# Optimization experiments

Measured on AMD Instinct MI355X. Metric: run time of the kernel, lower is better.

Reference implementation:

```python
import jax, jax.numpy as jnp
import numpy as np

H = 8          # num query heads
KV = 1         # num kv heads
D = 256        # head_dim
HID = 2048     # hidden_size
B = 4          # sequences in prefill batch
S = 2048       # tokens per sequence
T = B * S      # total tokens
NUM_SLOTS = 16384
ROPE_THETA = 10000.0


def setup_inputs() -> dict:
    key = jax.random.key(0)
    k1, k2, k3 = jax.random.split(key, 3)
    hidden_states = jax.random.normal(k1, (T, HID), dtype=jnp.float32)
    # real rotary tables: positions 0..S-1 repeated per sequence
    pos = jnp.tile(jnp.arange(S, dtype=jnp.float32), B)              # [T]
    inv_freq = 1.0 / (ROPE_THETA ** (jnp.arange(0, D, 2, dtype=jnp.float32) / D))  # [D/2]
    ang = pos[:, None] * inv_freq[None, :]                            # [T, D/2]
    cos, sin = jnp.cos(ang), jnp.sin(ang)
    slots = jnp.arange(T, dtype=jnp.int32)                            # contiguous slot mapping
    key_cache = jnp.zeros((NUM_SLOTS, KV, D), dtype=jnp.float32)
    value_cache = jnp.zeros((NUM_SLOTS, KV, D), dtype=jnp.float32)
    w_qkv = jax.random.normal(k2, ((H + 2 * KV) * D, HID), dtype=jnp.float32) * (HID ** -0.5)
    w_o = jax.random.normal(k3, (HID, H * D), dtype=jnp.float32) * ((H * D) ** -0.5)
    return {"hidden_states": hidden_states, "cos": cos, "sin": sin, "slots": slots,
            "key_cache": key_cache, "value_cache": value_cache, "w_qkv": w_qkv, "w_o": w_o}


def _rope(x, cos, sin):
    # rotate-half convention: x:[T, h, D], cos/sin:[T, D/2]
    x1, x2 = x[..., : D // 2], x[..., D // 2 :]
    c, s = cos[:, None, :], sin[:, None, :]
    return jnp.concatenate([x1 * c - x2 * s, x2 * c + x1 * s], axis=-1)


def reference(hidden_states, cos, sin, slots, key_cache, value_cache, w_qkv, w_o):
    qkv = hidden_states @ w_qkv.T                                  # [T, (H+2KV)*D]
    q = qkv[:, : H * D].reshape(T, H, D)
    k = qkv[:, H * D : (H + KV) * D].reshape(T, KV, D)
    v = qkv[:, (H + KV) * D :].reshape(T, KV, D)
    q = _rope(q, cos, sin)
    k = _rope(k, cos, sin)
    # paged_attention.reshape_and_cache: scatter post-RoPE k and raw v into cache slots
    key_cache = key_cache.at[slots].set(k)
    value_cache = value_cache.at[slots].set(v)
    # prefill flash attention: causal, per-sequence (equal-length ragged batch)
    qb = q.reshape(B, S, H, D)
    kb = jnp.repeat(k.reshape(B, S, KV, D), H // KV, axis=2)       # GQA expand
    vb = jnp.repeat(v.reshape(B, S, KV, D), H // KV, axis=2)
    scale = D ** -0.5
    scores = jnp.einsum("bqhd,bkhd->bhqk", qb, kb) * scale          # [B,H,S,S]
    causal = jnp.tril(jnp.ones((S, S), dtype=bool))
    scores = jnp.where(causal[None, None], scores, jnp.finfo(scores.dtype).min)
    probs = jax.nn.softmax(scores, axis=-1)
    attn = jnp.einsum("bhqk,bkhd->bqhd", probs, vb).reshape(T, H * D)
    out = attn @ w_o.T                                              # [T, HID]
    return out, key_cache, value_cache
```

## Files before the change

### kernel.cpp

```cpp
#include <hip/hip_runtime.h>

#define HN 8
#define DH 256
#define HID 2048
#define BB 4
#define SS 2048
#define TT (BB*SS)
#define NQKV 2560
#define NSLOTS 16384

typedef unsigned short u16;
typedef unsigned int u32;
typedef __bf16 bf16x8 __attribute__((ext_vector_type(8)));
typedef float f32x4 __attribute__((ext_vector_type(4)));
typedef u16 u16x4 __attribute__((ext_vector_type(4)));
typedef u16 u16x8 __attribute__((ext_vector_type(8)));

__device__ __forceinline__ u16 f2bf(float f) {
    u32 u = __builtin_bit_cast(u32, f);
    u = u + 0x7fffu + ((u >> 16) & 1u);
    return (u16)(u >> 16);
}
__device__ __forceinline__ float bf2f(u16 h) {
    u32 u = ((u32)h) << 16;
    return __builtin_bit_cast(float, u);
}
__device__ __forceinline__ void gload_lds16(const void* g, void* l) {
    __builtin_amdgcn_global_load_lds((__attribute__((address_space(1))) void*)g,
                                     (__attribute__((address_space(3))) void*)l,
                                     16, 0, 0);
}

__global__ __launch_bounds__(256) void cvt_f32_bf16(const float* __restrict__ in,
                                                    u16* __restrict__ out, long n) {
    long i = ((long)blockIdx.x * blockDim.x + threadIdx.x) * 4;
    long stride = (long)gridDim.x * blockDim.x * 4;
    for (; i < n; i += stride) {
        float4 v = *(const float4*)(in + i);
        u16x4 o4;
        o4[0] = f2bf(v.x); o4[1] = f2bf(v.y); o4[2] = f2bf(v.z); o4[3] = f2bf(v.w);
        *(u16x4*)(out + i) = o4;
    }
}

template<int OUTBF>
__global__ __launch_bounds__(256) void gemm_nt(const u16* __restrict__ A, const u16* __restrict__ B,
                                               void* __restrict__ C, int M, int N, int K) {
    __shared__ u16 As[128 * 32];
    __shared__ u16 Bs[128 * 32];
    const int tid = threadIdx.x;
    const int lane = tid & 63, w = tid >> 6;
    const int quad = lane >> 4, m16 = lane & 15;
    const int wm = w & 1, wn = w >> 1;
    const int r4 = tid >> 2, c8 = (tid & 3) * 8;
    const long arow = (long)blockIdx.x * 128;
    const long brow = (long)blockIdx.y * 128;

    f32x4 acc[4][4];
#pragma unroll
    for (int i = 0; i < 4; i++)
#pragma unroll
        for (int j = 0; j < 4; j++) acc[i][j] = (f32x4){0.f, 0.f, 0.f, 0.f};

    const u16* Ag = A + (arow + r4) * (long)K + c8;
    const u16* Bg = B + (brow + r4) * (long)K + c8;

    for (int k0 = 0; k0 < K; k0 += 32) {
        __syncthreads();
        gload_lds16(Ag + k0,                 (char*)As + tid * 16);
        gload_lds16(Ag + 64l * K + k0,       (char*)As + 4096 + tid * 16);
        gload_lds16(Bg + k0,                 (char*)Bs + tid * 16);
        gload_lds16(Bg + 64l * K + k0,       (char*)Bs + 4096 + tid * 16);
        __syncthreads();
        bf16x8 af[4], bfr[4];
#pragma unroll
        for (int mi = 0; mi < 4; mi++)
            af[mi] = *(const bf16x8*)(As + (wm * 64 + mi * 16 + m16) * 32 + quad * 8);
#pragma unroll
        for (int ni = 0; ni < 4; ni++)
            bfr[ni] = *(const bf16x8*)(Bs + (wn * 64 + ni * 16 + m16) * 32 + quad * 8);
#pragma unroll
        for (int mi = 0; mi < 4; mi++)
#pragma unroll
            for (int ni = 0; ni < 4; ni++)
                acc[mi][ni] = __builtin_amdgcn_mfma_f32_16x16x32_bf16(af[mi], bfr[ni], acc[mi][ni], 0, 0, 0);
    }
#pragma unroll
    for (int mi = 0; mi < 4; mi++) {
#pragma unroll
        for (int ni = 0; ni < 4; ni++) {
            long col = brow + wn * 64 + ni * 16 + m16;
#pragma unroll
            for (int r = 0; r < 4; r++) {
                long row = arow + wm * 64 + mi * 16 + quad * 4 + r;
                float v = acc[mi][ni][r];
                if (OUTBF) ((u16*)C)[row * N + col] = f2bf(v);
                else       ((float*)C)[row * N + col] = v;
            }
        }
    }
}

__global__ __launch_bounds__(256) void rope_scatter(u16* __restrict__ qkv, const float* __restrict__ cosb,
        const float* __restrict__ sinb, const int* __restrict__ slots,
        u16* __restrict__ kb, float* __restrict__ kc, float* __restrict__ vc) {
    const int t = blockIdx.x, tid = threadIdx.x;
    const long qbase = (long)t * NQKV;
#pragma unroll
    for (int i = 0; i < 4; i++) {
        int idx = tid + i * 256;
        int head = idx >> 7, d = idx & 127;
        long off = qbase + head * DH + d;
        float q1 = bf2f(qkv[off]), q2 = bf2f(qkv[off + 128]);
        float c = cosb[(long)t * 128 + d], s = sinb[(long)t * 128 + d];
        qkv[off]       = f2bf((q1 * c - q2 * s) * 0.0625f);
        qkv[off + 128] = f2bf((q2 * c + q1 * s) * 0.0625f);
    }
    const int slot = slots[t];
    if (tid < 128) {
        int d = tid;
        long off = qbase + HN * DH + d;
        float k1 = bf2f(qkv[off]), k2 = bf2f(qkv[off + 128]);
        float c = cosb[(long)t * 128 + d], s = sinb[(long)t * 128 + d];
        float kn1 = k1 * c - k2 * s, kn2 = k2 * c + k1 * s;
        kb[(long)t * DH + d]       = f2bf(kn1);
        kb[(long)t * DH + d + 128] = f2bf(kn2);
        kc[(long)slot * DH + d]       = kn1;
        kc[(long)slot * DH + d + 128] = kn2;
    }
    {
        int d = tid;
        vc[(long)slot * DH + d] = bf2f(qkv[qbase + (HN + 1) * DH + d]);
    }
}

__global__ __launch_bounds__(256) void transpose_v(const u16* __restrict__ qkv, u16* __restrict__ vbt) {
    const int tid = threadIdx.x;
    const int s0 = blockIdx.x * 64, d0 = blockIdx.y * 64, b = blockIdx.z;
#pragma unroll
    for (int i = 0; i < 2; i++) {
        int d = d0 + i * 32 + (tid >> 3);
        int s = s0 + (tid & 7) * 8;
        u16x8 v;
#pragma unroll
        for (int e = 0; e < 8; e++)
            v[e] = qkv[(long)(b * SS + s + e) * NQKV + (HN + 1) * DH + d];
        *(u16x8*)(vbt + ((long)b * DH + d) * SS + s) = v;
    }
}

__global__ __launch_bounds__(256, 4) void flash_attn(const u16* __restrict__ qkv, const u16* __restrict__ kb,
                                                     const u16* __restrict__ vbt, u16* __restrict__ attn) {
    __shared__ u16 Ks[32 * 256];
    __shared__ u16 Vt[256 * 32];
    __shared__ u16 Pl[4 * 16 * 40];
    const int tid = threadIdx.x;
    const int lane = tid & 63, w = tid >> 6;
    const int quad = lane >> 4, m16 = lane & 15;
    const int xr = blockIdx.x & 7, xt = blockIdx.x >> 3;
    const int qb = (xt == 0) ? 31 - xr : (xt == 1) ? 16 + xr : (xt == 2) ? 15 - xr : xr;
    const int h = blockIdx.y, b = blockIdx.z;
    const int qrow_w = qb * 64 + w * 16;

    const int krow = tid >> 5, kg = tid & 31, kgs = kg ^ krow;
    const int vrow = tid >> 2, vg = tid & 3,  vgs = vg ^ ((vrow >> 1) & 3);
    const int km7 = m16 & 7;
    const int vcol = (quad ^ ((m16 >> 1) & 3)) * 8;

    bf16x8 aq[8];
    {
        const u16* qp = qkv + (long)(b * SS + qrow_w + m16) * NQKV + h * DH;
#pragma unroll
        for (int ks = 0; ks < 8; ks++)
            aq[ks] = *(const bf16x8*)(qp + ks * 32 + quad * 8);
    }
    f32x4 o[16];
#pragma unroll
    for (int i = 0; i < 16; i++) o[i] = (f32x4){0.f, 0.f, 0.f, 0.f};
    float m_run[4] = {-1e30f, -1e30f, -1e30f, -1e30f};
    float l_run[4] = {0.f, 0.f, 0.f, 0.f};
    const long kvrow0 = (long)b * SS;
    const u16* vbase = vbt + (long)b * DH * SS;
    const int ntiles = 2 * qb + 2;

    for (int it = 0; it < ntiles; it++) {
        const int kv0 = it * 32;
        __syncthreads();
#pragma unroll
        for (int i = 0; i < 4; i++) {
            gload_lds16(kb + (kvrow0 + kv0 + i * 8 + krow) * DH + kgs * 8,
                        (char*)Ks + i * 4096 + tid * 16);
            gload_lds16(vbase + (long)(i * 64 + vrow) * SS + kv0 + vgs * 8,
                        (char*)Vt + i * 4096 + tid * 16);
        }
        asm volatile("s_waitcnt vmcnt(0)" ::: "memory");
        __syncthreads();

        f32x4 sc[2];
        sc[0] = (f32x4){0.f, 0.f, 0.f, 0.f};
        sc[1] = (f32x4){0.f, 0.f, 0.f, 0.f};
        __builtin_amdgcn_s_setprio(1);
#pragma unroll
        for (int ks = 0; ks < 8; ks++)
#pragma unroll
            for (int n = 0; n < 2; n++) {
                bf16x8 kf = *(const bf16x8*)(Ks + (n * 16 + m16) * 256 + (((ks * 4 + quad) ^ km7) << 3));
                sc[n] = __builtin_amdgcn_mfma_f32_16x16x32_bf16(aq[ks], kf, sc[n], 0, 0, 0);
            }
        __builtin_amdgcn_s_setprio(0);
        if (kv0 >= qb * 64) {
            const int qg = qrow_w + quad * 4;
#pragma unroll
            for (int n = 0; n < 2; n++) {
                int kvg = kv0 + n * 16 + m16;
#pragma unroll
                for (int r = 0; r < 4; r++)
                    if (kvg > qg + r) sc[n][r] = -1e30f;
            }
        }
        float mx[4];
#pragma unroll
        for (int r = 0; r < 4; r++) mx[r] = fmaxf(sc[0][r], sc[1][r]);
        bool grow = false;
#pragma unroll
        for (int r = 0; r < 4; r++) grow = grow || (mx[r] > m_run[r] + 8.f);
        if (__any((int)grow)) {
#pragma unroll
            for (int off = 1; off <= 8; off <<= 1)
#pragma unroll
                for (int r = 0; r < 4; r++) mx[r] = fmaxf(mx[r], __shfl_xor(mx[r], off));
#pragma unroll
            for (int r = 0; r < 4; r++) {
                float mn = fmaxf(m_run[r], mx[r]);
                float alpha = __expf(m_run[r] - mn);
                m_run[r] = mn;
                l_run[r] *= alpha;
#pragma unroll
                for (int nf = 0; nf < 16; nf++) o[nf][r] *= alpha;
            }
        }
#pragma unroll
        for (int n = 0; n < 2; n++)
#pragma unroll
            for (int r = 0; r < 4; r++) {
                float p = __expf(sc[n][r] - m_run[r]);
                sc[n][r] = p;
                l_run[r] += p;
            }
#pragma unroll
        for (int n = 0; n < 2; n++)
#pragma unroll
            for (int r = 0; r < 4; r++)
                Pl[w * 640 + (quad * 4 + r) * 40 + n * 16 + m16] = f2bf(sc[n][r]);
        asm volatile("s_waitcnt lgkmcnt(0)" ::: "memory");
        __builtin_amdgcn_sched_barrier(0);
        bf16x8 ap = *(const bf16x8*)(Pl + w * 640 + m16 * 40 + quad * 8);
        __builtin_amdgcn_s_setprio(1);
#pragma unroll
        for (int nf = 0; nf < 16; nf++) {
            bf16x8 vf = *(const bf16x8*)(Vt + (nf * 16 + m16) * 32 + vcol);
            o[nf] = __builtin_amdgcn_mfma_f32_16x16x32_bf16(ap, vf, o[nf], 0, 0, 0);
        }
        __builtin_amdgcn_s_setprio(0);
    }
#pragma unroll
    for (int off = 1; off <= 8; off <<= 1)
#pragma unroll
        for (int r = 0; r < 4; r++) l_run[r] += __shfl_xor(l_run[r], off);
    float inv[4];
#pragma unroll
    for (int r = 0; r < 4; r++) inv[r] = 1.f / l_run[r];
#pragma unroll
    for (int nf = 0; nf < 16; nf++)
#pragma unroll
        for (int r = 0; r < 4; r++) {
            long row = (long)(b * SS + qrow_w + quad * 4 + r);
            attn[row * (HN * DH) + h * DH + nf * 16 + m16] = f2bf(o[nf][r] * inv[r]);
        }
}

extern "C" void kernel_launch(void* const* d_in, const int* in_sizes, int n_in,
                              void* d_out, int out_size, void* d_ws, size_t ws_size,
                              hipStream_t stream) {
    (void)in_sizes; (void)n_in; (void)out_size; (void)ws_size;
    const float* hidden = (const float*)d_in[0];
    const float* cosb   = (const float*)d_in[1];
    const float* sinb   = (const float*)d_in[2];
    const int*   slots  = (const int*)d_in[3];
    const float* kc_in  = (const float*)d_in[4];
    const float* vc_in  = (const float*)d_in[5];
    const float* w_qkv  = (const float*)d_in[6];
    const float* w_o    = (const float*)d_in[7];

    float* out    = (float*)d_out;
    float* kc_out = out + (size_t)TT * HID;
    float* vc_out = kc_out + (size_t)NSLOTS * DH;

    char* p = (char*)d_ws;
    u16* hid_b  = (u16*)p;  p += (size_t)TT * HID * 2;
    u16* wqkv_b = (u16*)p;  p += (size_t)NQKV * HID * 2;
    u16* wo_b   = (u16*)p;  p += (size_t)HID * HID * 2;
    u16* kb     = (u16*)p;  p += (size_t)TT * DH * 2;
    u16* vbt    = (u16*)p;  p += (size_t)TT * DH * 2;
    u16* attn_b = hid_b;
    u16* qkv_b  = (u16*)d_out;

    hipMemcpyAsync(kc_out, kc_in, (size_t)NSLOTS * DH * 4, hipMemcpyDeviceToDevice, stream);
    hipMemcpyAsync(vc_out, vc_in, (size_t)NSLOTS * DH * 4, hipMemcpyDeviceToDevice, stream);

    cvt_f32_bf16<<<dim3(2048), dim3(256), 0, stream>>>(hidden, hid_b, (long)TT * HID);
    cvt_f32_bf16<<<dim3(640),  dim3(256), 0, stream>>>(w_qkv, wqkv_b, (long)NQKV * HID);
    cvt_f32_bf16<<<dim3(512),  dim3(256), 0, stream>>>(w_o,   wo_b,   (long)HID * HID);

    gemm_nt<1><<<dim3(TT / 128, NQKV / 128), dim3(256), 0, stream>>>(hid_b, wqkv_b, qkv_b, TT, NQKV, HID);
    rope_scatter<<<dim3(TT), dim3(256), 0, stream>>>(qkv_b, cosb, sinb, slots, kb, kc_out, vc_out);
    transpose_v<<<dim3(SS / 64, DH / 64, BB), dim3(256), 0, stream>>>(qkv_b, vbt);
    flash_attn<<<dim3(SS / 64, HN, BB), dim3(256), 0, stream>>>(qkv_b, kb, vbt, attn_b);
    gemm_nt<0><<<dim3(TT / 128, HID / 128), dim3(256), 0, stream>>>(attn_b, wo_b, out, TT, HID, HID);
}
```

Before: 656.0 us.

## Double-buffer K/V tiles and process 128-row query blocks with two fragments per wave

Flash attention now gives each wave 32 query rows as two 16-row fragments, so one K/V tile load from shared memory feeds twice the MFMA work. K and V tiles are double-buffered, and the next tile's global-to-LDS load is issued before computing on the current one. Per-wave causal skipping is added for tiles past the diagonal. The cost is higher register pressure (launch bounds drop to 2 blocks per SM), half as many blocks, and coarser load balance across the causal triangle.

```diff
diff --git a/kernel.cpp b/kernel.cpp
--- a/kernel.cpp
+++ b/kernel.cpp
@@ -149,134 +149,179 @@
     }
 }
 
-__global__ __launch_bounds__(256, 4) void flash_attn(const u16* __restrict__ qkv, const u16* __restrict__ kb,
+__global__ __launch_bounds__(256, 2) void flash_attn(const u16* __restrict__ qkv, const u16* __restrict__ kb,
                                                      const u16* __restrict__ vbt, u16* __restrict__ attn) {
-    __shared__ u16 Ks[32 * 256];
-    __shared__ u16 Vt[256 * 32];
-    __shared__ u16 Pl[4 * 16 * 40];
+    __shared__ u16 Ks[2][32 * 256];
+    __shared__ u16 Vt[2][256 * 32];
+    __shared__ u16 Pl[4 * 32 * 40];
     const int tid = threadIdx.x;
     const int lane = tid & 63, w = tid >> 6;
     const int quad = lane >> 4, m16 = lane & 15;
-    const int xr = blockIdx.x & 7, xt = blockIdx.x >> 3;
-    const int qb = (xt == 0) ? 31 - xr : (xt == 1) ? 16 + xr : (xt == 2) ? 15 - xr : xr;
+    const int x = blockIdx.x;
+    const int qb = (x < 8) ? x : 23 - x;
     const int h = blockIdx.y, b = blockIdx.z;
-    const int qrow_w = qb * 64 + w * 16;
+    const int qrow_w = qb * 128 + w * 32;
 
     const int krow = tid >> 5, kg = tid & 31, kgs = kg ^ krow;
     const int vrow = tid >> 2, vg = tid & 3,  vgs = vg ^ ((vrow >> 1) & 3);
     const int km7 = m16 & 7;
     const int vcol = (quad ^ ((m16 >> 1) & 3)) * 8;
 
-    bf16x8 aq[8];
-    {
-        const u16* qp = qkv + (long)(b * SS + qrow_w + m16) * NQKV + h * DH;
+    bf16x8 aq[2][8];
+#pragma unroll
+    for (int rf = 0; rf < 2; rf++) {
+        const u16* qp = qkv + (long)(b * SS + qrow_w + rf * 16 + m16) * NQKV + h * DH;
 #pragma unroll
         for (int ks = 0; ks < 8; ks++)
-            aq[ks] = *(const bf16x8*)(qp + ks * 32 + quad * 8);
-    }
-    f32x4 o[16];
-#pragma unroll
-    for (int i = 0; i < 16; i++) o[i] = (f32x4){0.f, 0.f, 0.f, 0.f};
-    float m_run[4] = {-1e30f, -1e30f, -1e30f, -1e30f};
-    float l_run[4] = {0.f, 0.f, 0.f, 0.f};
+            aq[rf][ks] = *(const bf16x8*)(qp + ks * 32 + quad * 8);
+    }
+    f32x4 o[2][16];
+#pragma unroll
+    for (int rf = 0; rf < 2; rf++)
+#pragma unroll
+        for (int i = 0; i < 16; i++) o[rf][i] = (f32x4){0.f, 0.f, 0.f, 0.f};
+    float m_run[2][4], l_run[2][4];
+#pragma unroll
+    for (int rf = 0; rf < 2; rf++)
+#pragma unroll
+        for (int r = 0; r < 4; r++) { m_run[rf][r] = -1e30f; l_run[rf][r] = 0.f; }
+
     const long kvrow0 = (long)b * SS;
     const u16* vbase = vbt + (long)b * DH * SS;
-    const int ntiles = 2 * qb + 2;
-
+    const int ntiles = 4 * qb + 4;
+
+    auto STAGE = [&](int bufi, int kv0_) {
+#pragma unroll
+        for (int i = 0; i < 4; i++) {
+            gload_lds16(kb + (kvrow0 + kv0_ + i * 8 + krow) * DH + kgs * 8,
+                        (char*)Ks[bufi] + i * 4096 + tid * 16);
+            gload_lds16(vbase + (long)(i * 64 + vrow) * SS + kv0_ + vgs * 8,
+                        (char*)Vt[bufi] + i * 4096 + tid * 16);
+        }
+    };
+
+    STAGE(0, 0);
     for (int it = 0; it < ntiles; it++) {
         const int kv0 = it * 32;
+        const int cur = it & 1;
+        if (it + 1 < ntiles) {
+            STAGE(cur ^ 1, kv0 + 32);
+            asm volatile("s_waitcnt vmcnt(8)" ::: "memory");
+        } else {
+            asm volatile("s_waitcnt vmcnt(0)" ::: "memory");
+        }
         __syncthreads();
-#pragma unroll
-        for (int i = 0; i < 4; i++) {
-            gload_lds16(kb + (kvrow0 + kv0 + i * 8 + krow) * DH + kgs * 8,
-                        (char*)Ks + i * 4096 + tid * 16);
-            gload_lds16(vbase + (long)(i * 64 + vrow) * SS + kv0 + vgs * 8,
-                        (char*)Vt + i * 4096 + tid * 16);
+
+        if (kv0 <= qrow_w + 31) {
+            const u16* Ksb = Ks[cur];
+            const u16* Vtb = Vt[cur];
+            f32x4 sc[2][2];
+#pragma unroll
+            for (int rf = 0; rf < 2; rf++)
+#pragma unroll
+                for (int n = 0; n < 2; n++) sc[rf][n] = (f32x4){0.f, 0.f, 0.f, 0.f};
+            __builtin_amdgcn_s_setprio(1);
+#pragma unroll
+            for (int ks = 0; ks < 8; ks++)
+#pragma unroll
+                for (int n = 0; n < 2; n++) {
+                    bf16x8 kf = *(const bf16x8*)(Ksb + (n * 16 + m16) * 256 + (((ks * 4 + quad) ^ km7) << 3));
+                    sc[0][n] = __builtin_amdgcn_mfma_f32_16x16x32_bf16(aq[0][ks], kf, sc[0][n], 0, 0, 0);
+                    sc[1][n] = __builtin_amdgcn_mfma_f32_16x16x32_bf16(aq[1][ks], kf, sc[1][n], 0, 0, 0);
+                }
+            __builtin_amdgcn_s_setprio(0);
+            if (kv0 >= qrow_w) {
+#pragma unroll
+                for (int rf = 0; rf < 2; rf++) {
+                    const int qg = qrow_w + rf * 16 + quad * 4;
+#pragma unroll
+                    for (int n = 0; n < 2; n++) {
+                        int kvg = kv0 + n * 16 + m16;
+#pragma unroll
+                        for (int r = 0; r < 4; r++)
+                            if (kvg > qg + r) sc[rf][n][r] = -1e30f;
+                    }
+                }
+            }
+            float mx[2][4];
+            bool grow = false;
+#pragma unroll
+            for (int rf = 0; rf < 2; rf++)
+#pragma unroll
+                for (int r = 0; r < 4; r++) {
+                    mx[rf][r] = fmaxf(sc[rf][0][r], sc[rf][1][r]);
+                    grow = grow || (mx[rf][r] > m_run[rf][r] + 8.f);
+                }
+            if (__any((int)grow)) {
+#pragma unroll
+                for (int off = 1; off <= 8; off <<= 1)
+#pragma unroll
+                    for (int rf = 0; rf < 2; rf++)
+#pragma unroll
+                        for (int r = 0; r < 4; r++) mx[rf][r] = fmaxf(mx[rf][r], __shfl_xor(mx[rf][r], off));
+#pragma unroll
+                for (int rf = 0; rf < 2; rf++)
+#pragma unroll
+                    for (int r = 0; r < 4; r++) {
+                        float mn = fmaxf(m_run[rf][r], mx[rf][r]);
+                        float alpha = __expf(m_run[rf][r] - mn);
+                        m_run[rf][r] = mn;
+                        l_run[rf][r] *= alpha;
+#pragma unroll
+                        for (int nf = 0; nf < 16; nf++) o[rf][nf][r] *= alpha;
+                    }
+            }
+#pragma unroll
+            for (int rf = 0; rf < 2; rf++)
+#pragma unroll
+                for (int n = 0; n < 2; n++)
+#pragma unroll
+                    for (int r = 0; r < 4; r++) {
+                        float p = __expf(sc[rf][n][r] - m_run[rf][r]);
+                        sc[rf][n][r] = p;
+                        l_run[rf][r] += p;
+                    }
+#pragma unroll
+            for (int rf = 0; rf < 2; rf++)
+#pragma unroll
+                for (int n = 0; n < 2; n++)
+#pragma unroll
+                    for (int r = 0; r < 4; r++)
+                        Pl[w * 1280 + (rf * 16 + quad * 4 + r) * 40 + n * 16 + m16] = f2bf(sc[rf][n][r]);
+            asm volatile("s_waitcnt lgkmcnt(0)" ::: "memory");
+            __builtin_amdgcn_sched_barrier(0);
+            bf16x8 ap0 = *(const bf16x8*)(Pl + w * 1280 + m16 * 40 + quad * 8);
+            bf16x8 ap1 = *(const bf16x8*)(Pl + w * 1280 + (16 + m16) * 40 + quad * 8);
+            __builtin_amdgcn_s_setprio(1);
+#pragma unroll
+            for (int nf = 0; nf < 16; nf++) {
+                bf16x8 vf = *(const bf16x8*)(Vtb + (nf * 16 + m16) * 32 + vcol);
+                o[0][nf] = __builtin_amdgcn_mfma_f32_16x16x32_bf16(ap0, vf, o[0][nf], 0, 0, 0);
+                o[1][nf] = __builtin_amdgcn_mfma_f32_16x16x32_bf16(ap1, vf, o[1][nf], 0, 0, 0);
+            }
+            __builtin_amdgcn_s_setprio(0);
         }
-        asm volatile("s_waitcnt vmcnt(0)" ::: "memory");
         __syncthreads();
-
-        f32x4 sc[2];
-        sc[0] = (f32x4){0.f, 0.f, 0.f, 0.f};
-        sc[1] = (f32x4){0.f, 0.f, 0.f, 0.f};
-        __builtin_amdgcn_s_setprio(1);
-#pragma unroll
-        for (int ks = 0; ks < 8; ks++)
-#pragma unroll
-            for (int n = 0; n < 2; n++) {
-                bf16x8 kf = *(const bf16x8*)(Ks + (n * 16 + m16) * 256 + (((ks * 4 + quad) ^ km7) << 3));
-                sc[n] = __builtin_amdgcn_mfma_f32_16x16x32_bf16(aq[ks], kf, sc[n], 0, 0, 0);
-            }
-        __builtin_amdgcn_s_setprio(0);
-        if (kv0 >= qb * 64) {
-            const int qg = qrow_w + quad * 4;
-#pragma unroll
-            for (int n = 0; n < 2; n++) {
-                int kvg = kv0 + n * 16 + m16;
-#pragma unroll
-                for (int r = 0; r < 4; r++)
-                    if (kvg > qg + r) sc[n][r] = -1e30f;
-            }
-        }
-        float mx[4];
-#pragma unroll
-        for (int r = 0; r < 4; r++) mx[r] = fmaxf(sc[0][r], sc[1][r]);
-        bool grow = false;
-#pragma unroll
-        for (int r = 0; r < 4; r++) grow = grow || (mx[r] > m_run[r] + 8.f);
-        if (__any((int)grow)) {
-#pragma unroll
-            for (int off = 1; off <= 8; off <<= 1)
-#pragma unroll
-                for (int r = 0; r < 4; r++) mx[r] = fmaxf(mx[r], __shfl_xor(mx[r], off));
+    }
+#pragma unroll
+    for (int off = 1; off <= 8; off <<= 1)
+#pragma unroll
+        for (int rf = 0; rf < 2; rf++)
+#pragma unroll
+            for (int r = 0; r < 4; r++) l_run[rf][r] += __shfl_xor(l_run[rf][r], off);
+#pragma unroll
+    for (int rf = 0; rf < 2; rf++) {
+        float inv[4];
+#pragma unroll
+        for (int r = 0; r < 4; r++) inv[r] = 1.f / l_run[rf][r];
+#pragma unroll
+        for (int nf = 0; nf < 16; nf++)
 #pragma unroll
             for (int r = 0; r < 4; r++) {
-                float mn = fmaxf(m_run[r], mx[r]);
-                float alpha = __expf(m_run[r] - mn);
-                m_run[r] = mn;
-                l_run[r] *= alpha;
-#pragma unroll
-                for (int nf = 0; nf < 16; nf++) o[nf][r] *= alpha;
-            }
-        }
-#pragma unroll
-        for (int n = 0; n < 2; n++)
-#pragma unroll
-            for (int r = 0; r < 4; r++) {
-                float p = __expf(sc[n][r] - m_run[r]);
-                sc[n][r] = p;
-                l_run[r] += p;
-            }
-#pragma unroll
-        for (int n = 0; n < 2; n++)
-#pragma unroll
-            for (int r = 0; r < 4; r++)
-                Pl[w * 640 + (quad * 4 + r) * 40 + n * 16 + m16] = f2bf(sc[n][r]);
-        asm volatile("s_waitcnt lgkmcnt(0)" ::: "memory");
-        __builtin_amdgcn_sched_barrier(0);
-        bf16x8 ap = *(const bf16x8*)(Pl + w * 640 + m16 * 40 + quad * 8);
-        __builtin_amdgcn_s_setprio(1);
-#pragma unroll
-        for (int nf = 0; nf < 16; nf++) {
-            bf16x8 vf = *(const bf16x8*)(Vt + (nf * 16 + m16) * 32 + vcol);
-            o[nf] = __builtin_amdgcn_mfma_f32_16x16x32_bf16(ap, vf, o[nf], 0, 0, 0);
-        }
-        __builtin_amdgcn_s_setprio(0);
-    }
-#pragma unroll
-    for (int off = 1; off <= 8; off <<= 1)
-#pragma unroll
-        for (int r = 0; r < 4; r++) l_run[r] += __shfl_xor(l_run[r], off);
-    float inv[4];
-#pragma unroll
-    for (int r = 0; r < 4; r++) inv[r] = 1.f / l_run[r];
-#pragma unroll
-    for (int nf = 0; nf < 16; nf++)
-#pragma unroll
-        for (int r = 0; r < 4; r++) {
-            long row = (long)(b * SS + qrow_w + quad * 4 + r);
-            attn[row * (HN * DH) + h * DH + nf * 16 + m16] = f2bf(o[nf][r] * inv[r]);
-        }
+                long row = (long)(b * SS + qrow_w + rf * 16 + quad * 4 + r);
+                attn[row * (HN * DH) + h * DH + nf * 16 + m16] = f2bf(o[rf][nf][r] * inv[r]);
+            }
+    }
 }
 
 extern "C" void kernel_launch(void* const* d_in, const int* in_sizes, int n_in,
@@ -315,6 +360,6 @@
     gemm_nt<1><<<dim3(TT / 128, NQKV / 128), dim3(256), 0, stream>>>(hid_b, wqkv_b, qkv_b, TT, NQKV, HID);
     rope_scatter<<<dim3(TT), dim3(256), 0, stream>>>(qkv_b, cosb, sinb, slots, kb, kc_out, vc_out);
     transpose_v<<<dim3(SS / 64, DH / 64, BB), dim3(256), 0, stream>>>(qkv_b, vbt);
-    flash_attn<<<dim3(SS / 64, HN, BB), dim3(256), 0, stream>>>(qkv_b, kb, vbt, attn_b);
+    flash_attn<<<dim3(SS / 128, HN, BB), dim3(256), 0, stream>>>(qkv_b, kb, vbt, attn_b);
     gemm_nt<0><<<dim3(TT / 128, HID / 128), dim3(256), 0, stream>>>(attn_b, wo_b, out, TT, HID, HID);
 }
```

Measured after the change: 692.2 us. 1.06x slower.

## Compute transposed S tile so P stays in registers, skip masked tiles

Applied to the files above, without the earlier changes.

Swaps the MFMA operand order so each lane holds scores for one query row across eight keys. The K rows are permuted on load so that this register layout matches the A-operand layout of the P·V MFMA. That removes the LDS round-trip for P and lets the row max and sum use fewer shuffles. Each wave also skips key tiles that lie entirely above its own causal diagonal. In exchange the K-row permutation and lane mapping have to be exactly right for the result to stay correct.

```diff
diff --git a/kernel.cpp b/kernel.cpp
--- a/kernel.cpp
+++ b/kernel.cpp
@@ -29,6 +29,11 @@
     __builtin_amdgcn_global_load_lds((__attribute__((address_space(1))) void*)g,
                                      (__attribute__((address_space(3))) void*)l,
                                      16, 0, 0);
+}
+__device__ __forceinline__ u32 cvtpk_bf16(float a, float b) {
+    u32 r;
+    asm("v_cvt_pk_bf16_f32 %0, %1, %2" : "=v"(r) : "v"(a), "v"(b));
+    return r;
 }
 
 __global__ __launch_bounds__(256) void cvt_f32_bf16(const float* __restrict__ in,
@@ -153,7 +158,6 @@
                                                      const u16* __restrict__ vbt, u16* __restrict__ attn) {
     __shared__ u16 Ks[32 * 256];
     __shared__ u16 Vt[256 * 32];
-    __shared__ u16 Pl[4 * 16 * 40];
     const int tid = threadIdx.x;
     const int lane = tid & 63, w = tid >> 6;
     const int quad = lane >> 4, m16 = lane & 15;
@@ -163,6 +167,7 @@
     const int qrow_w = qb * 64 + w * 16;
 
     const int krow = tid >> 5, kg = tid & 31, kgs = kg ^ krow;
+    const int ks_hi = (krow >> 2) << 3, ks_lo = krow & 3;
     const int vrow = tid >> 2, vg = tid & 3,  vgs = vg ^ ((vrow >> 1) & 3);
     const int km7 = m16 & 7;
     const int vcol = (quad ^ ((m16 >> 1) & 3)) * 8;
@@ -177,8 +182,8 @@
     f32x4 o[16];
 #pragma unroll
     for (int i = 0; i < 16; i++) o[i] = (f32x4){0.f, 0.f, 0.f, 0.f};
-    float m_run[4] = {-1e30f, -1e30f, -1e30f, -1e30f};
-    float l_run[4] = {0.f, 0.f, 0.f, 0.f};
+    float m_run = -1e30f;
+    float l_run = 0.f;
     const long kvrow0 = (long)b * SS;
     const u16* vbase = vbt + (long)b * DH * SS;
     const int ntiles = 2 * qb + 2;
@@ -188,7 +193,8 @@
         __syncthreads();
 #pragma unroll
         for (int i = 0; i < 4; i++) {
-            gload_lds16(kb + (kvrow0 + kv0 + i * 8 + krow) * DH + kgs * 8,
+            const int srcrow = ((i & 1) << 4) + ks_hi + ((i >> 1) << 2) + ks_lo;
+            gload_lds16(kb + (kvrow0 + kv0 + srcrow) * DH + kgs * 8,
                         (char*)Ks + i * 4096 + tid * 16);
             gload_lds16(vbase + (long)(i * 64 + vrow) * SS + kv0 + vgs * 8,
                         (char*)Vt + i * 4096 + tid * 16);
@@ -196,86 +202,79 @@
         asm volatile("s_waitcnt vmcnt(0)" ::: "memory");
         __syncthreads();
 
-        f32x4 sc[2];
-        sc[0] = (f32x4){0.f, 0.f, 0.f, 0.f};
-        sc[1] = (f32x4){0.f, 0.f, 0.f, 0.f};
-        __builtin_amdgcn_s_setprio(1);
-#pragma unroll
-        for (int ks = 0; ks < 8; ks++)
-#pragma unroll
-            for (int n = 0; n < 2; n++) {
-                bf16x8 kf = *(const bf16x8*)(Ks + (n * 16 + m16) * 256 + (((ks * 4 + quad) ^ km7) << 3));
-                sc[n] = __builtin_amdgcn_mfma_f32_16x16x32_bf16(aq[ks], kf, sc[n], 0, 0, 0);
+        if (kv0 <= qrow_w + 15) {
+            f32x4 sc[2];
+            sc[0] = (f32x4){0.f, 0.f, 0.f, 0.f};
+            sc[1] = (f32x4){0.f, 0.f, 0.f, 0.f};
+            __builtin_amdgcn_s_setprio(1);
+#pragma unroll
+            for (int ks = 0; ks < 8; ks++)
+#pragma unroll
+                for (int n = 0; n < 2; n++) {
+                    bf16x8 kf = *(const bf16x8*)(Ks + (n * 16 + m16) * 256 + (((ks * 4 + quad) ^ km7) << 3));
+                    sc[n] = __builtin_amdgcn_mfma_f32_16x16x32_bf16(kf, aq[ks], sc[n], 0, 0, 0);
+                }
+            __builtin_amdgcn_s_setprio(0);
+            if (kv0 >= qb * 64) {
+                const int qg = qrow_w + m16;
+                const int kvb = kv0 + quad * 8;
+#pragma unroll
+                for (int n = 0; n < 2; n++)
+#pragma unroll
+                    for (int r = 0; r < 4; r++)
+                        if (kvb + n * 4 + r > qg) sc[n][r] = -1e30f;
             }
-        __builtin_amdgcn_s_setprio(0);
-        if (kv0 >= qb * 64) {
-            const int qg = qrow_w + quad * 4;
-#pragma unroll
-            for (int n = 0; n < 2; n++) {
-                int kvg = kv0 + n * 16 + m16;
-#pragma unroll
-                for (int r = 0; r < 4; r++)
-                    if (kvg > qg + r) sc[n][r] = -1e30f;
+            float mx = fmaxf(fmaxf(fmaxf(sc[0][0], sc[0][1]), fmaxf(sc[0][2], sc[0][3])),
+                             fmaxf(fmaxf(sc[1][0], sc[1][1]), fmaxf(sc[1][2], sc[1][3])));
+            if (__any((int)(mx > m_run + 8.f))) {
+                float mr = fmaxf(mx, __shfl_xor(mx, 16));
+                mr = fmaxf(mr, __shfl_xor(mr, 32));
+                float mn = fmaxf(m_run, mr);
+                float alpha = __expf(m_run - mn);
+                m_run = mn;
+                l_run *= alpha;
+                float ar[4];
+#pragma unroll
+                for (int r = 0; r < 4; r++) ar[r] = __shfl(alpha, quad * 4 + r);
+#pragma unroll
+                for (int nf = 0; nf < 16; nf++)
+#pragma unroll
+                    for (int r = 0; r < 4; r++) o[nf][r] *= ar[r];
             }
+#pragma unroll
+            for (int n = 0; n < 2; n++)
+#pragma unroll
+                for (int r = 0; r < 4; r++) {
+                    float p = __expf(sc[n][r] - m_run);
+                    sc[n][r] = p;
+                    l_run += p;
+                }
+            union { u32 w4[4]; bf16x8 v; } pu;
+            pu.w4[0] = cvtpk_bf16(sc[0][0], sc[0][1]);
+            pu.w4[1] = cvtpk_bf16(sc[0][2], sc[0][3]);
+            pu.w4[2] = cvtpk_bf16(sc[1][0], sc[1][1]);
+            pu.w4[3] = cvtpk_bf16(sc[1][2], sc[1][3]);
+            __builtin_amdgcn_s_setprio(1);
+#pragma unroll
+            for (int nf = 0; nf < 16; nf++) {
+                bf16x8 vf = *(const bf16x8*)(Vt + (nf * 16 + m16) * 32 + vcol);
+                o[nf] = __builtin_amdgcn_mfma_f32_16x16x32_bf16(pu.v, vf, o[nf], 0, 0, 0);
+            }
+            __builtin_amdgcn_s_setprio(0);
         }
-        float mx[4];
-#pragma unroll
-        for (int r = 0; r < 4; r++) mx[r] = fmaxf(sc[0][r], sc[1][r]);
-        bool grow = false;
-#pragma unroll
-        for (int r = 0; r < 4; r++) grow = grow || (mx[r] > m_run[r] + 8.f);
-        if (__any((int)grow)) {
-#pragma unroll
-            for (int off = 1; off <= 8; off <<= 1)
-#pragma unroll
-                for (int r = 0; r < 4; r++) mx[r] = fmaxf(mx[r], __shfl_xor(mx[r], off));
-#pragma unroll
-            for (int r = 0; r < 4; r++) {
-                float mn = fmaxf(m_run[r], mx[r]);
-                float alpha = __expf(m_run[r] - mn);
-                m_run[r] = mn;
-                l_run[r] *= alpha;
-#pragma unroll
-                for (int nf = 0; nf < 16; nf++) o[nf][r] *= alpha;
-            }
-        }
-#pragma unroll
-        for (int n = 0; n < 2; n++)
-#pragma unroll
-            for (int r = 0; r < 4; r++) {
-                float p = __expf(sc[n][r] - m_run[r]);
-                sc[n][r] = p;
-                l_run[r] += p;
-            }
-#pragma unroll
-        for (int n = 0; n < 2; n++)
-#pragma unroll
-            for (int r = 0; r < 4; r++)
-                Pl[w * 640 + (quad * 4 + r) * 40 + n * 16 + m16] = f2bf(sc[n][r]);
-        asm volatile("s_waitcnt lgkmcnt(0)" ::: "memory");
-        __builtin_amdgcn_sched_barrier(0);
-        bf16x8 ap = *(const bf16x8*)(Pl + w * 640 + m16 * 40 + quad * 8);
-        __builtin_amdgcn_s_setprio(1);
-#pragma unroll
-        for (int nf = 0; nf < 16; nf++) {
-            bf16x8 vf = *(const bf16x8*)(Vt + (nf * 16 + m16) * 32 + vcol);
-            o[nf] = __builtin_amdgcn_mfma_f32_16x16x32_bf16(ap, vf, o[nf], 0, 0, 0);
-        }
-        __builtin_amdgcn_s_setprio(0);
-    }
-#pragma unroll
-    for (int off = 1; off <= 8; off <<= 1)
-#pragma unroll
-        for (int r = 0; r < 4; r++) l_run[r] += __shfl_xor(l_run[r], off);
-    float inv[4];
-#pragma unroll
-    for (int r = 0; r < 4; r++) inv[r] = 1.f / l_run[r];
+    }
+    l_run += __shfl_xor(l_run, 16);
+    l_run += __shfl_xor(l_run, 32);
+    float invm = 1.f / l_run;
+    float ir[4];
+#pragma unroll
+    for (int r = 0; r < 4; r++) ir[r] = __shfl(invm, quad * 4 + r);
 #pragma unroll
     for (int nf = 0; nf < 16; nf++)
 #pragma unroll
         for (int r = 0; r < 4; r++) {
             long row = (long)(b * SS + qrow_w + quad * 4 + r);
-            attn[row * (HN * DH) + h * DH + nf * 16 + m16] = f2bf(o[nf][r] * inv[r]);
+            attn[row * (HN * DH) + h * DH + nf * 16 + m16] = f2bf(o[nf][r] * ir[r]);
         }
 }
 
```

Result: no change. 646.4 us (-1.5%).
